# Optimization experiments

Measured on AMD Instinct MI355X. Metric: run time of the kernel, lower is better.

## Reference

```python
import jax, jax.numpy as jnp
from jax import lax
import numpy as np

PROPRIO = 48
NPTS = 1024
NP_PROX = 512
NP_DIST = 512
HP = 187  # proximal_feature_dim
HD = 64   # distal_feature_dim
B = 2048
NA = 12
ACTOR_DIMS = [PROPRIO + HP + HD, 1024, 512, 256, 128, NA]


def gru_last(x, wih, whh, bih, bhh):
    """torch-style GRU (gate order r,z,n), returns last hidden. x: [B,T,in]."""
    Bx, T, _ = x.shape
    H = whh.shape[1]
    gx = x @ wih.T + bih  # [B,T,3H], input projections precomputed
    def step(h, gxt):
        gh = h @ whh.T + bhh
        r = jax.nn.sigmoid(gxt[:, :H] + gh[:, :H])
        z = jax.nn.sigmoid(gxt[:, H:2 * H] + gh[:, H:2 * H])
        n = jnp.tanh(gxt[:, 2 * H:] + r * gh[:, 2 * H:])
        return (1.0 - z) * n + z * h, None
    h0 = jnp.zeros((Bx, H), x.dtype)
    hT, _ = lax.scan(step, h0, jnp.swapaxes(gx, 0, 1))
    return hT


def _encode(pts, w1, b1, w2, b2):
    h = jax.nn.elu(pts @ w1.T + b1)
    return jax.nn.elu(h @ w2.T + b2)


def _forward(obs, pe_prox_w1, pe_prox_b1, pe_prox_w2, pe_prox_b2,
             pe_dist_w1, pe_dist_b1, pe_dist_w2, pe_dist_b2,
             gru_prox_wih, gru_prox_whh, gru_prox_bih, gru_prox_bhh,
             gru_dist_wih, gru_dist_whh, gru_dist_bih, gru_dist_bhh,
             mem_prox_wih, mem_prox_whh, mem_prox_bih, mem_prox_bhh,
             mem_dist_wih, mem_dist_whh, mem_dist_bih, mem_dist_bhh,
             actor_w0, actor_b0, actor_w1, actor_b1, actor_w2, actor_b2,
             actor_w3, actor_b3, actor_w4, actor_b4,
             prox_idx, dist_idx):
    proprio = obs[:, :PROPRIO]
    lidar = obs[:, PROPRIO:].reshape(obs.shape[0], NPTS, 3)  # history_length=1
    # irregular gather of proximal/distal point subsets (sampling plan buffers)
    prox_enc = _encode(lidar[:, prox_idx], pe_prox_w1, pe_prox_b1, pe_prox_w2, pe_prox_b2)  # [B,512,64]
    dist_enc = _encode(lidar[:, dist_idx], pe_dist_w1, pe_dist_b1, pe_dist_w2, pe_dist_b2)  # [B,512,64]
    # spatial GRUs over the point sequence
    hp = gru_last(prox_enc, gru_prox_wih, gru_prox_whh, gru_prox_bih, gru_prox_bhh)  # [B,187]
    hd = gru_last(dist_enc, gru_dist_wih, gru_dist_whh, gru_dist_bih, gru_dist_bhh)  # [B,64]
    # temporal memory GRUs (single step, zero initial hidden)
    fp = gru_last(hp[:, None, :], mem_prox_wih, mem_prox_whh, mem_prox_bih, mem_prox_bhh)
    fd = gru_last(hd[:, None, :], mem_dist_wih, mem_dist_whh, mem_dist_bih, mem_dist_bhh)
    x = jnp.concatenate([proprio, fp, fd], axis=-1)  # [B,299]
    for w, b in ((actor_w0, actor_b0), (actor_w1, actor_b1), (actor_w2, actor_b2), (actor_w3, actor_b3)):
        x = jax.nn.elu(x @ w.T + b)
    return x @ actor_w4.T + actor_b4  # action mean [B,12]


def setup_inputs() -> dict:
    key = jax.random.key(0)
    ks = iter(jax.random.split(key, 64))
    def n(shape, scale=0.05):
        return (jax.random.normal(next(ks), shape, jnp.float32) * scale)
    inp = {}
    inp["obs"] = jax.random.normal(next(ks), (B, PROPRIO + NPTS * 3), jnp.float32)
    inp["prox_idx"] = jax.random.randint(next(ks), (NP_PROX,), 0, NPTS)
    inp["dist_idx"] = jax.random.randint(next(ks), (NP_DIST,), 0, NPTS)
    for pfx in ("pe_prox", "pe_dist"):
        inp[pfx + "_w1"] = n((64, 3)); inp[pfx + "_b1"] = jnp.zeros((64,), jnp.float32)
        inp[pfx + "_w2"] = n((64, 64)); inp[pfx + "_b2"] = jnp.zeros((64,), jnp.float32)
    for pfx, H, din in (("gru_prox", HP, 64), ("gru_dist", HD, 64), ("mem_prox", HP, HP), ("mem_dist", HD, HD)):
        inp[pfx + "_wih"] = n((3 * H, din)); inp[pfx + "_whh"] = n((3 * H, H))
        inp[pfx + "_bih"] = jnp.zeros((3 * H,), jnp.float32); inp[pfx + "_bhh"] = jnp.zeros((3 * H,), jnp.float32)
    for i, (di, do) in enumerate(zip(ACTOR_DIMS[:-1], ACTOR_DIMS[1:])):
        inp[f"actor_w{i}"] = n((do, di)); inp[f"actor_b{i}"] = jnp.zeros((do,), jnp.float32)
    return inp


def reference(obs, prox_idx, dist_idx,
              pe_prox_w1, pe_prox_b1, pe_prox_w2, pe_prox_b2,
              pe_dist_w1, pe_dist_b1, pe_dist_w2, pe_dist_b2,
              gru_prox_wih, gru_prox_whh, gru_prox_bih, gru_prox_bhh,
              gru_dist_wih, gru_dist_whh, gru_dist_bih, gru_dist_bhh,
              mem_prox_wih, mem_prox_whh, mem_prox_bih, mem_prox_bhh,
              mem_dist_wih, mem_dist_whh, mem_dist_bih, mem_dist_bhh,
              actor_w0, actor_b0, actor_w1, actor_b1, actor_w2, actor_b2,
              actor_w3, actor_b3, actor_w4, actor_b4):
    return _forward(obs, pe_prox_w1, pe_prox_b1, pe_prox_w2, pe_prox_b2,
                    pe_dist_w1, pe_dist_b1, pe_dist_w2, pe_dist_b2,
                    gru_prox_wih, gru_prox_whh, gru_prox_bih, gru_prox_bhh,
                    gru_dist_wih, gru_dist_whh, gru_dist_bih, gru_dist_bhh,
                    mem_prox_wih, mem_prox_whh, mem_prox_bih, mem_prox_bhh,
                    mem_dist_wih, mem_dist_whh, mem_dist_bih, mem_dist_bhh,
                    actor_w0, actor_b0, actor_w1, actor_b1, actor_w2, actor_b2,
                    actor_w3, actor_b3, actor_w4, actor_b4,
                    prox_idx, dist_idx)
```

## Files before the change

kernel.cpp:

```cpp
#include <hip/hip_runtime.h>
#include <stdint.h>

typedef __attribute__((ext_vector_type(8))) short short8;
typedef __attribute__((ext_vector_type(4))) float f32x4;
typedef __attribute__((ext_vector_type(4))) unsigned int u32x4;

#define DEV __device__ __forceinline__

#define L2E 1.4426950408889634f

DEV unsigned short f2bf(float f) {
    union { float f; uint32_t u; } v; v.f = f;
    return (unsigned short)((v.u + 0x7FFFu + ((v.u >> 16) & 1u)) >> 16);
}
#if defined(__has_builtin)
#if __has_builtin(__builtin_amdgcn_cvt_pk_bf16_f32)
#define HAS_PK_BF16 1
#endif
#if __has_builtin(__builtin_amdgcn_cvt_pk_fp8_f32)
#define HAS_PK_FP8 1
#endif
#endif
DEV uint32_t pk_bf16(float a, float b) {
#ifdef HAS_PK_BF16
    typedef __attribute__((ext_vector_type(2))) __bf16 bf2;
    union { bf2 v; uint32_t u; } cv;
    cv.v = __builtin_amdgcn_cvt_pk_bf16_f32(a, b);
    return cv.u;
#else
    return (uint32_t)f2bf(a) | ((uint32_t)f2bf(b) << 16);
#endif
}
DEV uint8_t f2fp8(float f) {
    union { float f; uint32_t u; } v; v.f = f;
    uint32_t s = (v.u >> 24) & 0x80u;
    uint32_t absu = v.u & 0x7FFFFFFFu;
    int E = (int)(absu >> 23);
    if (E >= 136) return (uint8_t)(s | 0x7E);
    if (E >= 121) {
        uint32_t m = absu & 0x7FFFFFu;
        uint32_t keep = m >> 20;
        uint32_t rest = m & 0xFFFFFu;
        uint32_t rnd = (rest > 0x80000u || (rest == 0x80000u && (keep & 1u))) ? 1u : 0u;
        uint32_t mag = (((uint32_t)(E - 120) << 3) | keep) + rnd;
        if (mag > 0x7Eu) mag = 0x7Eu;
        return (uint8_t)(s | mag);
    }
    float sc = __builtin_fabsf(f) * 512.f;
    uint32_t m8 = (uint32_t)(sc + 0.5f);
    if (m8 > 7u) return (uint8_t)(s | 0x08);
    return (uint8_t)(s | m8);
}
DEV uint32_t pk_fp8x4(float a, float b, float c, float d) {
#ifdef HAS_PK_FP8
    int lo   = __builtin_amdgcn_cvt_pk_fp8_f32(a, b, 0, false);
    int both = __builtin_amdgcn_cvt_pk_fp8_f32(c, d, lo, true);
    return (uint32_t)both;
#else
    return (uint32_t)f2fp8(a) | ((uint32_t)f2fp8(b) << 8)
         | ((uint32_t)f2fp8(c) << 16) | ((uint32_t)f2fp8(d) << 24);
#endif
}
DEV float rcp1pe_(float x) {
    return __builtin_amdgcn_rcpf(1.f + __builtin_amdgcn_exp2f(x));
}
DEV float sig_(float x) { return rcp1pe_(-L2E * x); }
DEV float elu_(float x) {
    return x > 0.f ? x : __builtin_amdgcn_exp2f(L2E * x) - 1.f;
}
DEV f32x4 splat4(float v) { f32x4 r; r[0]=v; r[1]=v; r[2]=v; r[3]=v; return r; }
DEV void pin(short8& v) { asm volatile("" : "+v"(v)); }
DEV void pinl(long& v)  { asm volatile("" : "+v"(v)); }

struct PJob { const float* s; void* d; int Hs, NG, Ks, Kd, total; float s0, s1, s2; int fmt; };
struct PJobs { PJob j[13]; };

__global__ __launch_bounds__(256) void pack_all(PJobs P)
{
    PJob jb = P.j[blockIdx.y];
    int e = blockIdx.x * 256 + threadIdx.x;
    if (e >= jb.total) return;
    int n = e / jb.Kd, k = e - n * jb.Kd;
    int g = n / jb.NG, jj = n - g * jb.NG;
    float sc = (g == 0) ? jb.s0 : ((g == 1) ? jb.s1 : jb.s2);
    float v = (jj < jb.Hs && k < jb.Ks) ? jb.s[(size_t)(g * jb.Hs + jj) * jb.Ks + k] * sc : 0.f;
    if (jb.fmt) ((uint8_t*)jb.d)[e] = (uint8_t)(pk_fp8x4(v, 0.f, 0.f, 0.f) & 0xFFu);
    else        ((unsigned short*)jb.d)[e] = f2bf(v);
}

__global__ __launch_bounds__(256) void enc_kernel(
    const float* __restrict__ obs, const int* __restrict__ idx,
    const float* __restrict__ w1, const float* __restrict__ b1,
    const unsigned short* __restrict__ w2p, const float* __restrict__ b2,
    uint8_t* __restrict__ enc8)
{
    const int b = blockIdx.x, t0 = blockIdx.y * 64;
    const int tid = threadIdx.x;
    __shared__ __align__(16) float pts[64][4];
    __shared__ float w1s[256];
    __shared__ float b1s[64], b2s[64];
    __shared__ __align__(16) unsigned short h1s[64][72];
    __shared__ __align__(16) uint8_t x8s[64 * 80];

    if (tid < 192) w1s[(tid/3)*4 + (tid - (tid/3)*3)] = w1[tid];
    if (tid < 64) { b1s[tid] = b1[tid]; b2s[tid] = b2[tid]; }
    for (int e = tid; e < 192; e += 256) {
        int p = e / 3, c2 = e - p * 3;
        int pi = idx[t0 + p];
        pts[p][c2] = obs[(size_t)b * 3120 + 48 + (size_t)pi * 3 + c2];
    }
    __syncthreads();
#pragma unroll
    for (int r = 0; r < 16; ++r) {
        int e = tid + r * 256;
        int p = e >> 6, ch = e & 63;
        float v = w1s[ch*4]*pts[p][0] + w1s[ch*4+1]*pts[p][1]
                + w1s[ch*4+2]*pts[p][2] + b1s[ch];
        h1s[p][ch] = f2bf(elu_(v));
    }
    __syncthreads();
    const int wave = tid >> 6, lane = tid & 63, quad = lane >> 4, l16 = lane & 15;
#pragma unroll
    for (int ct = 0; ct < 4; ++ct) {
        f32x4 a2 = splat4(0.f);
#pragma unroll
        for (int ks = 0; ks < 2; ++ks) {
            short8 af = *(const short8*)(&h1s[wave*16 + l16][ks*32 + quad*8]);
            short8 bf = *(const short8*)(w2p + (ct*16 + l16)*64 + ks*32 + quad*8);
            a2 = __builtin_amdgcn_mfma_f32_16x16x32_bf16(af, bf, a2, 0, 0, 0);
        }
        int c = ct*16 + l16;
        float b2v = b2s[c];
        uint32_t pk = pk_fp8x4(elu_(a2[0] + b2v), elu_(a2[1] + b2v),
                               elu_(a2[2] + b2v), elu_(a2[3] + b2v));
#pragma unroll
        for (int j = 0; j < 4; ++j)
            x8s[(wave*16 + quad*4 + j)*80 + c] = (uint8_t)(pk >> (8*j));
    }
    __syncthreads();
    {
        int row = tid >> 2, seg = tid & 3;
        *(u32x4*)(enc8 + ((size_t)b*512 + t0 + row)*64 + seg*16) =
            *(const u32x4*)(x8s + row*80 + seg*16);
    }
}

DEV void gru_body_pre(int blk, const uint8_t* __restrict__ enc8,
                      const uint8_t* __restrict__ wih8,
                      const unsigned short* __restrict__ whh,
                      const float* __restrict__ bih, const float* __restrict__ bhh,
                      unsigned short* __restrict__ houtb, char* smem)
{
    constexpr int H = 187, KP = 192, KS = 6, HP8 = 200;
    unsigned short* hlds = (unsigned short*)smem;
    uint8_t* xs = (uint8_t*)(smem + 12800);

    const int tid  = threadIdx.x;
    const int wave = tid >> 6, lane = tid & 63, quad = lane >> 4, l16 = lane & 15;
    const int b0   = blk * 16;
    const int c    = wave * 16 + l16;

    const int sx = (l16 >> 2) & 3;
    const int qo = (quad ^ sx) * 8;
    const int cc = c >> 3, cl = c & 7;
    const int wcol = ((cc & ~3) | ((cc & 3) ^ quad)) * 8 + cl;

    for (int e = tid; e < 2*16*HP8; e += 768) hlds[e] = 0;

    short8 whr[3][KS];
    long   wx8[3][2];
#pragma unroll
    for (int g = 0; g < 3; ++g) {
#pragma unroll
        for (int ks = 0; ks < KS; ++ks)
            whr[g][ks] = *(const short8*)(whh + ((size_t)(g*KP + c))*KP + ks*32 + quad*8);
#pragma unroll
        for (int ks = 0; ks < 2; ++ks)
            wx8[g][ks] = *(const long*)(wih8 + ((size_t)(g*KP + c))*64 + ks*32 + quad*8);
    }
#pragma unroll
    for (int g = 0; g < 3; ++g) {
#pragma unroll
        for (int ks = 0; ks < KS; ++ks) pin(whr[g][ks]);
#pragma unroll
        for (int ks = 0; ks < 2; ++ks)  pinl(wx8[g][ks]);
    }
    float bsr = 0.f, bsz = 0.f, binx = 0.f, bhnn = 0.f;
    if (c < H) {
        bsr  = -L2E * (bih[c]       + bhh[c]);
        bsz  = -L2E * (bih[H + c]   + bhh[H + c]);
        binx = 2.f * L2E * bih[2*H + c];
        bhnn = 2.f * L2E * bhh[2*H + c];
    }
    float hreg[4] = {0.f, 0.f, 0.f, 0.f};

    u32x4 xq;
    const int xrow = lane >> 2, xseg = lane & 3;
    if (wave == 0) {
        xq = *(const u32x4*)(enc8 + ((size_t)(b0 + xrow)*512 + 0)*64 + xseg*16);
        *(u32x4*)(xs + 0*1280 + xrow*80 + xseg*16) = xq;
        xq = *(const u32x4*)(enc8 + ((size_t)(b0 + xrow)*512 + 1)*64 + xseg*16);
    }
    __syncthreads();

    int cur = 0;
    for (int t = 0; t < 512; ++t) {
        if (wave == 0) {
            *(u32x4*)(xs + ((t+1)&1)*1280 + xrow*80 + xseg*16) = xq;
            int tn = (t + 2 < 512) ? t + 2 : 511;
            xq = *(const u32x4*)(enc8 + ((size_t)(b0 + xrow)*512 + tn)*64 + xseg*16);
        }
        const uint8_t* xsr = xs + (t&1)*1280;
        const unsigned short* hc = hlds + cur * (16*HP8);
        unsigned short*       hn = hlds + (cur ^ 1) * (16*HP8);

        f32x4 acc[4];
        acc[0] = splat4(bsr);
        acc[1] = splat4(bsz);
        acc[2] = splat4(binx);
        acc[3] = splat4(bhnn);
#pragma unroll
        for (int ks = 0; ks < 2; ++ks) {
            long a8 = *(const long*)(xsr + l16*80 + ks*32 + quad*8);
            acc[0] = __builtin_amdgcn_mfma_f32_16x16x32_fp8_fp8(a8, wx8[0][ks], acc[0], 0, 0, 0);
            acc[1] = __builtin_amdgcn_mfma_f32_16x16x32_fp8_fp8(a8, wx8[1][ks], acc[1], 0, 0, 0);
            acc[2] = __builtin_amdgcn_mfma_f32_16x16x32_fp8_fp8(a8, wx8[2][ks], acc[2], 0, 0, 0);
        }
#pragma unroll
        for (int ks = 0; ks < KS; ++ks) {
            short8 ah = *(const short8*)(hc + l16*HP8 + ks*32 + qo);
            acc[0] = __builtin_amdgcn_mfma_f32_16x16x32_bf16(ah, whr[0][ks], acc[0], 0, 0, 0);
            acc[1] = __builtin_amdgcn_mfma_f32_16x16x32_bf16(ah, whr[1][ks], acc[1], 0, 0, 0);
            acc[3] = __builtin_amdgcn_mfma_f32_16x16x32_bf16(ah, whr[2][ks], acc[3], 0, 0, 0);
        }
        float hv[4];
#pragma unroll
        for (int j = 0; j < 4; ++j) {
            float r  = rcp1pe_(acc[0][j]);
            float zg = rcp1pe_(acc[1][j]);
            float nn = __builtin_fmaf(-2.f, rcp1pe_(__builtin_fmaf(r, acc[3][j], acc[2][j])), 1.f);
            hv[j] = __builtin_fmaf(zg, hreg[j] - nn, nn);
            hreg[j] = hv[j];
        }
        uint32_t p01 = pk_bf16(hv[0], hv[1]);
        uint32_t p23 = pk_bf16(hv[2], hv[3]);
        hn[(quad*4+0)*HP8 + wcol] = (unsigned short)p01;
        hn[(quad*4+1)*HP8 + wcol] = (unsigned short)(p01 >> 16);
        hn[(quad*4+2)*HP8 + wcol] = (unsigned short)p23;
        hn[(quad*4+3)*HP8 + wcol] = (unsigned short)(p23 >> 16);
        cur ^= 1;
        __syncthreads();
    }
#pragma unroll
    for (int j = 0; j < 4; ++j) {
        int m = quad*4 + j;
        houtb[(size_t)(b0 + m)*KP + c] = (c < H) ? f2bf(hreg[j]) : 0;
    }
}

template<int H, int KP>
DEV void gru_body_fused(int blk,
                  const float* __restrict__ obs, const int* __restrict__ idx,
                  const float* __restrict__ w1, const float* __restrict__ b1,
                  const float* __restrict__ w2, const float* __restrict__ b2,
                  const unsigned short* __restrict__ wih, const unsigned short* __restrict__ whh,
                  const float* __restrict__ bih, const float* __restrict__ bhh,
                  unsigned short* __restrict__ houtb, char* smem)
{
    constexpr int NCT = KP / 16;
    constexpr int KS  = KP / 32;
    constexpr int HP8 = KP + 8;

    unsigned short* hlds = (unsigned short*)(smem);
    unsigned short* xs   = (unsigned short*)(smem + 12800);
    unsigned short* h1s  = (unsigned short*)(smem + 17408);
    unsigned short* w2s  = (unsigned short*)(smem + 22016);
    float* ptsb          = (float*)(smem + 31232);
    float* w1s           = (float*)(smem + 31744);
    float* b1s           = (float*)(smem + 32768);
    float* b2s           = (float*)(smem + 33024);

    const int tid  = threadIdx.x;
    const int wave = tid >> 6, lane = tid & 63, quad = lane >> 4, l16 = lane & 15;
    const int b0   = blk * 16;
    const int ct   = wave;
    const bool act = (ct < NCT);
    const int c    = ct * 16 + l16;

    for (int e = tid; e < 2*16*HP8; e += 768) hlds[e] = 0;
    for (int e = tid; e < 4096; e += 768) { int n = e >> 6, k = e & 63; w2s[n*72 + k] = f2bf(w2[e]); }
    if (tid < 192) w1s[(tid/3)*4 + (tid - (tid/3)*3)] = w1[tid];
    if (tid < 64) { b1s[tid] = b1[tid]; b2s[tid] = b2[tid]; }

    const float* myrow = obs + (size_t)(b0 + (tid & 15)) * 3120 + 48;
    float px = 0.f, py = 0.f, pz = 0.f;
    if (tid < 16) {
        int p0 = idx[0];
        ptsb[tid*4 + 0] = myrow[3*p0 + 0];
        ptsb[tid*4 + 1] = myrow[3*p0 + 1];
        ptsb[tid*4 + 2] = myrow[3*p0 + 2];
        int p1 = idx[1];
        px = myrow[3*p1 + 0]; py = myrow[3*p1 + 1]; pz = myrow[3*p1 + 2];
    }

    short8 whr[3][KS];
    short8 wxr[3][2];
    float bsr = 0.f, bsz = 0.f, binx = 0.f, bhnn = 0.f;
    {
        const int cl = act ? c : l16;
#pragma unroll
        for (int g = 0; g < 3; ++g) {
#pragma unroll
            for (int ks = 0; ks < KS; ++ks)
                whr[g][ks] = *(const short8*)(whh + ((size_t)(g*KP + cl))*KP + ks*32 + quad*8);
#pragma unroll
            for (int ks = 0; ks < 2; ++ks)
                wxr[g][ks] = *(const short8*)(wih + ((size_t)(g*KP + cl))*64 + ks*32 + quad*8);
        }
    }
#pragma unroll
    for (int g = 0; g < 3; ++g) {
#pragma unroll
        for (int ks = 0; ks < KS; ++ks) pin(whr[g][ks]);
#pragma unroll
        for (int ks = 0; ks < 2; ++ks)  pin(wxr[g][ks]);
    }
    if (act && c < H) {
        bsr  = -L2E * (bih[c]       + bhh[c]);
        bsz  = -L2E * (bih[H + c]   + bhh[H + c]);
        binx = 2.f * L2E * bih[2*H + c];
        bhnn = 2.f * L2E * bhh[2*H + c];
    }
    float hreg[4] = {0.f, 0.f, 0.f, 0.f};

    __syncthreads();

    int cur = 0;
    for (int i = 0; i < 514; ++i) {
        if (i < 512) {
            const float* pt = ptsb + (i & 1) * 64;
            unsigned short* h1w = h1s + (i & 1) * (16*72);
#pragma unroll
            for (int e = tid; e < 1024; e += 768) {
                int p = e >> 6, ch = e & 63;
                float v = w1s[ch*4+0]*pt[p*4+0] + w1s[ch*4+1]*pt[p*4+1]
                        + w1s[ch*4+2]*pt[p*4+2] + b1s[ch];
                h1w[p*72 + ch] = f2bf(elu_(v));
            }
            if (tid < 16) {
                float* dst = ptsb + ((i+1) & 1) * 64 + tid*4;
                dst[0] = px; dst[1] = py; dst[2] = pz;
                int tn = (i + 2 < 512) ? i + 2 : 511;
                int pn = idx[tn];
                px = myrow[3*pn + 0]; py = myrow[3*pn + 1]; pz = myrow[3*pn + 2];
            }
        }
        if (i >= 1 && i < 513 && wave < 4) {
            const unsigned short* h1r = h1s + ((i-1) & 1) * (16*72);
            unsigned short*       xw  = xs  + ((i-1) & 1) * (16*72);
            f32x4 a2 = splat4(0.f);
#pragma unroll
            for (int ks = 0; ks < 2; ++ks) {
                short8 af = *(const short8*)(h1r + l16*72 + ks*32 + quad*8);
                short8 bf = *(const short8*)(w2s + (wave*16 + l16)*72 + ks*32 + quad*8);
                a2 = __builtin_amdgcn_mfma_f32_16x16x32_bf16(af, bf, a2, 0, 0, 0);
            }
            int c2 = wave*16 + l16;
            float b2v = b2s[c2];
#pragma unroll
            for (int j = 0; j < 4; ++j)
                xw[(quad*4 + j)*72 + c2] = f2bf(elu_(a2[j] + b2v));
        }
        if (i >= 2) {
            int t = i - 2;
            const unsigned short* xsr = xs + (t & 1) * (16*72);
            const unsigned short* hc  = hlds + cur * (16*HP8);
            unsigned short*       hn  = hlds + (cur ^ 1) * (16*HP8);
            if (act) {
                f32x4 acc[4];
                acc[0] = splat4(bsr);
                acc[1] = splat4(bsz);
                acc[2] = splat4(binx);
                acc[3] = splat4(bhnn);
#pragma unroll
                for (int ks = 0; ks < 2; ++ks) {
                    short8 xf = *(const short8*)(xsr + l16*72 + ks*32 + quad*8);
                    acc[0] = __builtin_amdgcn_mfma_f32_16x16x32_bf16(xf, wxr[0][ks], acc[0], 0, 0, 0);
                    acc[1] = __builtin_amdgcn_mfma_f32_16x16x32_bf16(xf, wxr[1][ks], acc[1], 0, 0, 0);
                    acc[2] = __builtin_amdgcn_mfma_f32_16x16x32_bf16(xf, wxr[2][ks], acc[2], 0, 0, 0);
                }
#pragma unroll
                for (int ks = 0; ks < KS; ++ks) {
                    short8 ah = *(const short8*)(hc + l16*HP8 + ks*32 + quad*8);
                    acc[0] = __builtin_amdgcn_mfma_f32_16x16x32_bf16(ah, whr[0][ks], acc[0], 0, 0, 0);
                    acc[1] = __builtin_amdgcn_mfma_f32_16x16x32_bf16(ah, whr[1][ks], acc[1], 0, 0, 0);
                    acc[3] = __builtin_amdgcn_mfma_f32_16x16x32_bf16(ah, whr[2][ks], acc[3], 0, 0, 0);
                }
                float hv[4];
#pragma unroll
                for (int j = 0; j < 4; ++j) {
                    float r  = rcp1pe_(acc[0][j]);
                    float zg = rcp1pe_(acc[1][j]);
                    float nn = __builtin_fmaf(-2.f, rcp1pe_(__builtin_fmaf(r, acc[3][j], acc[2][j])), 1.f);
                    hv[j] = __builtin_fmaf(zg, hreg[j] - nn, nn);
                    hreg[j] = hv[j];
                }
                uint32_t p01 = pk_bf16(hv[0], hv[1]);
                uint32_t p23 = pk_bf16(hv[2], hv[3]);
                hn[(quad*4+0)*HP8 + c] = (unsigned short)p01;
                hn[(quad*4+1)*HP8 + c] = (unsigned short)(p01 >> 16);
                hn[(quad*4+2)*HP8 + c] = (unsigned short)p23;
                hn[(quad*4+3)*HP8 + c] = (unsigned short)(p23 >> 16);
            }
            cur ^= 1;
        }
        __syncthreads();
    }

    if (act)
#pragma unroll
        for (int j = 0; j < 4; ++j) {
            int m = quad*4 + j;
            houtb[(size_t)(b0 + m)*KP + c] = (c < H) ? f2bf(hreg[j]) : 0;
        }
}

__global__ __launch_bounds__(768) void gru_kernel(
    int mode,
    const float* __restrict__ obs,
    const int* __restrict__ prox_idx, const int* __restrict__ dist_idx,
    const uint8_t* __restrict__ encp8, const uint8_t* __restrict__ wihp8,
    const float* __restrict__ w1p, const float* __restrict__ b1p,
    const float* __restrict__ w2p, const float* __restrict__ b2p,
    const float* __restrict__ w1d, const float* __restrict__ b1d,
    const float* __restrict__ w2d, const float* __restrict__ b2d,
    const unsigned short* __restrict__ wihp, const unsigned short* __restrict__ whhp,
    const unsigned short* __restrict__ wihd, const unsigned short* __restrict__ whhd,
    const float* __restrict__ bihp, const float* __restrict__ bhhp,
    const float* __restrict__ bihd, const float* __restrict__ bhhd,
    unsigned short* __restrict__ hpb, unsigned short* __restrict__ hdb)
{
    __shared__ __align__(16) char smem[33280];
    if (blockIdx.x < 128) {
        if (mode == 0)
            gru_body_pre(blockIdx.x, encp8, wihp8, whhp, bihp, bhhp, hpb, smem);
        else
            gru_body_fused<187, 192>(blockIdx.x, obs, prox_idx, w1p, b1p, w2p, b2p,
                                     wihp, whhp, bihp, bhhp, hpb, smem);
    } else {
        gru_body_fused<64, 64>(blockIdx.x - 128, obs, dist_idx, w1d, b1d, w2d, b2d,
                               wihd, whhd, bihd, bhhd, hdb, smem);
    }
}

__global__ __launch_bounds__(256) void memfuse_kernel(
    const float* __restrict__ obs,
    const unsigned short* __restrict__ hpb, const unsigned short* __restrict__ hdb,
    const unsigned short* __restrict__ mwp, const unsigned short* __restrict__ mwd,
    const float* __restrict__ mbip, const float* __restrict__ mbhp,
    const float* __restrict__ mbid, const float* __restrict__ mbhd,
    unsigned short* __restrict__ x0b)
{
    __shared__ __align__(16) unsigned short Asl[64*40];
    __shared__ __align__(16) unsigned short Bsl[3][64*40];
    const int tid = threadIdx.x;
    const int wave = tid >> 6, lane = tid & 63, quad = lane >> 4, l16 = lane & 15;
    const int z = blockIdx.x, m0 = blockIdx.y * 64;
    const bool isp = (z < 3);
    const unsigned short* A = isp ? hpb : hdb;
    const unsigned short* B = isp ? mwp : mwd;
    const float* bi = isp ? mbip : mbid;
    const float* bh = isp ? mbhp : mbhd;
    const int Kp = isp ? 192 : 64;
    const int Hh = isp ? 187 : 64;
    const int jb = isp ? z * 64 : 0;
    const int cbase = isp ? 48 : 235;
    const int r = tid >> 2, sg = (tid & 3) * 8;

    f32x4 acc[3][4];
#pragma unroll
    for (int g = 0; g < 3; ++g)
#pragma unroll
        for (int nt = 0; nt < 4; ++nt) acc[g][nt] = splat4(0.f);

    for (int k0 = 0; k0 < Kp; k0 += 32) {
        *(short8*)(Asl + r*40 + sg) = *(const short8*)(A + (size_t)(m0 + r)*Kp + k0 + sg);
#pragma unroll
        for (int g = 0; g < 3; ++g)
            *(short8*)(Bsl[g] + r*40 + sg) =
                *(const short8*)(B + (size_t)(g*Kp + jb + r)*Kp + k0 + sg);
        __syncthreads();
        short8 af = *(const short8*)(Asl + (wave*16 + l16)*40 + quad*8);
#pragma unroll
        for (int g = 0; g < 3; ++g)
#pragma unroll
            for (int nt = 0; nt < 4; ++nt) {
                short8 bf = *(const short8*)(Bsl[g] + (nt*16 + l16)*40 + quad*8);
                acc[g][nt] = __builtin_amdgcn_mfma_f32_16x16x32_bf16(af, bf, acc[g][nt], 0, 0, 0);
            }
        __syncthreads();
    }
#pragma unroll
    for (int nt = 0; nt < 4; ++nt) {
        int j = jb + nt*16 + l16;
        bool valid = (j < Hh);
        float br = 0.f, bz = 0.f, bnx = 0.f, bnh = 0.f;
        if (valid) {
            br  = -L2E * (bi[j] + bh[j]);
            bz  = -L2E * (bi[Hh + j] + bh[Hh + j]);
            bnx = 2.f * L2E * bi[2*Hh + j];
            bnh = 2.f * L2E * bh[2*Hh + j];
        }
#pragma unroll
        for (int jj = 0; jj < 4; ++jj) {
            int m = m0 + wave*16 + quad*4 + jj;
            float rr = rcp1pe_(acc[0][nt][jj] + br);
            float zz = rcp1pe_(acc[1][nt][jj] + bz);
            float tt = __builtin_fmaf(rr, bnh, acc[2][nt][jj] + bnx);
            float nn = __builtin_fmaf(-2.f, rcp1pe_(tt), 1.f);
            float v  = (1.f - zz) * nn;
            if (valid) x0b[(size_t)m*320 + cbase + j] = f2bf(v);
        }
    }
    if (z == 0) {
        for (int e = tid; e < 64*48; e += 256) {
            int m = m0 + e / 48, cc = e - (e / 48) * 48;
            x0b[(size_t)m*320 + cc] = f2bf(obs[(size_t)m*3120 + cc]);
        }
    }
    if (z == 3) {
        for (int e = tid; e < 64*21; e += 256) {
            int m = m0 + e / 21, cc = 299 + (e - (e / 21) * 21);
            x0b[(size_t)m*320 + cc] = 0;
        }
    }
}

__global__ __launch_bounds__(256) void bgemm_kernel(
    const unsigned short* __restrict__ A, const unsigned short* __restrict__ B,
    const float* __restrict__ bias, void* __restrict__ C,
    int Kp, int Np, int Nstore, int mode)
{
    __shared__ __align__(16) unsigned short Asl[64*72];
    __shared__ __align__(16) unsigned short Bsl[64*72];
    const int tid = threadIdx.x;
    const int wave = tid >> 6, lane = tid & 63, quad = lane >> 4, l16 = lane & 15;
    const int n0 = blockIdx.x * 64, m0 = blockIdx.y * 64;
    const int r = tid >> 2, sg = (tid & 3) * 16;

    f32x4 acc[4];
#pragma unroll
    for (int nt = 0; nt < 4; ++nt) acc[nt] = splat4(0.f);

    for (int k0 = 0; k0 < Kp; k0 += 64) {
        *(short8*)(Asl + r*72 + sg)     = *(const short8*)(A + (size_t)(m0 + r)*Kp + k0 + sg);
        *(short8*)(Asl + r*72 + sg + 8) = *(const short8*)(A + (size_t)(m0 + r)*Kp + k0 + sg + 8);
        if (n0 + r < Np) {
            *(short8*)(Bsl + r*72 + sg)     = *(const short8*)(B + (size_t)(n0 + r)*Kp + k0 + sg);
            *(short8*)(Bsl + r*72 + sg + 8) = *(const short8*)(B + (size_t)(n0 + r)*Kp + k0 + sg + 8);
        } else {
            short8 zz; for (int q = 0; q < 8; ++q) zz[q] = 0;
            *(short8*)(Bsl + r*72 + sg) = zz;
            *(short8*)(Bsl + r*72 + sg + 8) = zz;
        }
        __syncthreads();
#pragma unroll
        for (int ks = 0; ks < 2; ++ks) {
            short8 af = *(const short8*)(Asl + (wave*16 + l16)*72 + ks*32 + quad*8);
#pragma unroll
            for (int nt = 0; nt < 4; ++nt) {
                short8 bf = *(const short8*)(Bsl + (nt*16 + l16)*72 + ks*32 + quad*8);
                acc[nt] = __builtin_amdgcn_mfma_f32_16x16x32_bf16(af, bf, acc[nt], 0, 0, 0);
            }
        }
        __syncthreads();
    }
#pragma unroll
    for (int nt = 0; nt < 4; ++nt) {
        int n = n0 + nt*16 + l16;
        float bv = (bias && n < Np) ? bias[n] : 0.f;
#pragma unroll
        for (int j = 0; j < 4; ++j) {
            int m = m0 + wave*16 + quad*4 + j;
            float v = acc[nt][j] + bv;
            if (mode == 1) {
                ((unsigned short*)C)[(size_t)m*Np + n] = f2bf(elu_(v));
            } else {
                if (n < Nstore) ((float*)C)[(size_t)m*Nstore + n] = v;
            }
        }
    }
}

__global__ __launch_bounds__(256) void gemm34_kernel(
    const unsigned short* __restrict__ A,
    const unsigned short* __restrict__ W3,
    const float* __restrict__ b3,
    const unsigned short* __restrict__ W4,
    const float* __restrict__ b4,
    float* __restrict__ out)
{
    __shared__ __align__(16) char smem[9216 + 18432];
    unsigned short* Asl  = (unsigned short*)smem;
    unsigned short* B3sl = (unsigned short*)(smem + 9216);
    unsigned short* a4s  = (unsigned short*)smem;
    const int tid = threadIdx.x;
    const int wave = tid >> 6, lane = tid & 63, quad = lane >> 4, l16 = lane & 15;
    const int m0 = blockIdx.x * 64;

    f32x4 acc3[8];
#pragma unroll
    for (int nt = 0; nt < 8; ++nt) acc3[nt] = splat4(0.f);

    const int r = tid >> 2, sg = (tid & 3) * 16;
    const int r2 = tid >> 1, sg2 = (tid & 1) * 32;
    for (int k0 = 0; k0 < 256; k0 += 64) {
        *(short8*)(Asl + r*72 + sg)     = *(const short8*)(A + (size_t)(m0 + r)*256 + k0 + sg);
        *(short8*)(Asl + r*72 + sg + 8) = *(const short8*)(A + (size_t)(m0 + r)*256 + k0 + sg + 8);
#pragma unroll
        for (int s = 0; s < 4; ++s)
            *(short8*)(B3sl + r2*72 + sg2 + s*8) =
                *(const short8*)(W3 + (size_t)r2*256 + k0 + sg2 + s*8);
        __syncthreads();
#pragma unroll
        for (int ks = 0; ks < 2; ++ks) {
            short8 af = *(const short8*)(Asl + (wave*16 + l16)*72 + ks*32 + quad*8);
#pragma unroll
            for (int nt = 0; nt < 8; ++nt) {
                short8 bf = *(const short8*)(B3sl + (nt*16 + l16)*72 + ks*32 + quad*8);
                acc3[nt] = __builtin_amdgcn_mfma_f32_16x16x32_bf16(af, bf, acc3[nt], 0, 0, 0);
            }
        }
        __syncthreads();
    }
#pragma unroll
    for (int nt = 0; nt < 8; ++nt) {
        int n = nt*16 + l16;
        float bv = b3[n];
#pragma unroll
        for (int j = 0; j < 4; ++j) {
            int m = wave*16 + quad*4 + j;
            a4s[m*136 + n] = f2bf(elu_(acc3[nt][j] + bv));
        }
    }
    __syncthreads();
    f32x4 acc4 = splat4(0.f);
#pragma unroll
    for (int ks = 0; ks < 4; ++ks) {
        short8 af = *(const short8*)(a4s + (wave*16 + l16)*136 + ks*32 + quad*8);
        short8 bf = *(const short8*)(W4 + (size_t)l16*128 + ks*32 + quad*8);
        acc4 = __builtin_amdgcn_mfma_f32_16x16x32_bf16(af, bf, acc4, 0, 0, 0);
    }
    if (l16 < 12) {
        float bv = b4[l16];
#pragma unroll
        for (int j = 0; j < 4; ++j)
            out[(size_t)(m0 + wave*16 + quad*4 + j)*12 + l16] = acc4[j] + bv;
    }
}

extern "C" void kernel_launch(void* const* d_in, const int* in_sizes, int n_in,
                              void* d_out, int out_size, void* d_ws, size_t ws_size,
                              hipStream_t stream)
{
    (void)in_sizes; (void)n_in; (void)out_size;
    const float* obs        = (const float*)d_in[0];
    const int*   prox_idx   = (const int*)d_in[1];
    const int*   dist_idx   = (const int*)d_in[2];
    const float* pe_prox_w1 = (const float*)d_in[3];
    const float* pe_prox_b1 = (const float*)d_in[4];
    const float* pe_prox_w2 = (const float*)d_in[5];
    const float* pe_prox_b2 = (const float*)d_in[6];
    const float* pe_dist_w1 = (const float*)d_in[7];
    const float* pe_dist_b1 = (const float*)d_in[8];
    const float* pe_dist_w2 = (const float*)d_in[9];
    const float* pe_dist_b2 = (const float*)d_in[10];
    const float* gp_wih = (const float*)d_in[11];
    const float* gp_whh = (const float*)d_in[12];
    const float* gp_bih = (const float*)d_in[13];
    const float* gp_bhh = (const float*)d_in[14];
    const float* gd_wih = (const float*)d_in[15];
    const float* gd_whh = (const float*)d_in[16];
    const float* gd_bih = (const float*)d_in[17];
    const float* gd_bhh = (const float*)d_in[18];
    const float* mp_wih = (const float*)d_in[19];
    const float* mp_bih = (const float*)d_in[21];
    const float* mp_bhh = (const float*)d_in[22];
    const float* md_wih = (const float*)d_in[23];
    const float* md_bih = (const float*)d_in[25];
    const float* md_bhh = (const float*)d_in[26];
    const float* aw0 = (const float*)d_in[27]; const float* ab0 = (const float*)d_in[28];
    const float* aw1 = (const float*)d_in[29]; const float* ab1 = (const float*)d_in[30];
    const float* aw2 = (const float*)d_in[31]; const float* ab2 = (const float*)d_in[32];
    const float* aw3 = (const float*)d_in[33]; const float* ab3 = (const float*)d_in[34];
    const float* aw4 = (const float*)d_in[35]; const float* ab4 = (const float*)d_in[36];
    float* out = (float*)d_out;

    char* ws = (char*)d_ws;
    size_t off = 0;
    auto alloc = [&](size_t bytes) -> char* {
        char* p = ws + off;
        off = (off + bytes + 255) & ~(size_t)255;
        return p;
    };
    unsigned short* wih_p = (unsigned short*)alloc(36864*2);
    unsigned short* whh_p = (unsigned short*)alloc(110592*2);
    unsigned short* wih_d = (unsigned short*)alloc(12288*2);
    unsigned short* whh_d = (unsigned short*)alloc(12288*2);
    unsigned short* mw_p  = (unsigned short*)alloc(110592*2);
    unsigned short* mw_d  = (unsigned short*)alloc(12288*2);
    unsigned short* w0p   = (unsigned short*)alloc((size_t)1024*320*2);
    unsigned short* w1p   = (unsigned short*)alloc((size_t)512*1024*2);
    unsigned short* w2p   = (unsigned short*)alloc((size_t)256*512*2);
    unsigned short* w3p   = (unsigned short*)alloc((size_t)128*256*2);
    unsigned short* w4p   = (unsigned short*)alloc((size_t)16*128*2);
    unsigned short* w2e   = (unsigned short*)alloc(4096*2);
    uint8_t* wih8         = (uint8_t*)alloc(576*64);
    unsigned short* hpb   = (unsigned short*)alloc((size_t)2048*192*2);
    unsigned short* hdb   = (unsigned short*)alloc((size_t)2048*64*2);
    unsigned short* x0b   = (unsigned short*)alloc((size_t)2048*320*2);
    unsigned short* a1b   = (unsigned short*)alloc((size_t)2048*1024*2);
    unsigned short* a2b   = (unsigned short*)alloc((size_t)2048*512*2);
    unsigned short* a3b   = (unsigned short*)alloc((size_t)2048*256*2);
    uint8_t* enc8         = (uint8_t*)alloc((size_t)2048*512*64);
    const int mode = (off <= ws_size) ? 0 : 1;

    const float SR = -L2E, SN = 2.f * L2E;
    PJobs P;
    P.j[0]  = { gp_wih, wih_p, 187, 192, 64, 64, 36864, SR, SR, SN, 0 };
    P.j[1]  = { gp_whh, whh_p, 187, 192, 187, 192, 110592, SR, SR, SN, 0 };
    P.j[2]  = { gd_wih, wih_d, 64, 64, 64, 64, 12288, SR, SR, SN, 0 };
    P.j[3]  = { gd_whh, whh_d, 64, 64, 64, 64, 12288, SR, SR, SN, 0 };
    P.j[4]  = { mp_wih, mw_p, 187, 192, 187, 192, 110592, SR, SR, SN, 0 };
    P.j[5]  = { md_wih, mw_d, 64, 64, 64, 64, 12288, SR, SR, SN, 0 };
    P.j[6]  = { aw0, w0p, 1024, 1024, 299, 320, 327680, 1.f, 1.f, 1.f, 0 };
    P.j[7]  = { aw1, w1p, 512, 512, 1024, 1024, 524288, 1.f, 1.f, 1.f, 0 };
    P.j[8]  = { aw2, w2p, 256, 256, 512, 512, 131072, 1.f, 1.f, 1.f, 0 };
    P.j[9]  = { aw3, w3p, 128, 128, 256, 256, 32768, 1.f, 1.f, 1.f, 0 };
    P.j[10] = { aw4, w4p, 12, 16, 128, 128, 2048, 1.f, 1.f, 1.f, 0 };
    P.j[11] = { pe_prox_w2, w2e, 64, 64, 64, 64, 4096, 1.f, 1.f, 1.f, 0 };
    P.j[12] = { gp_wih, wih8, 187, 192, 64, 64, 36864, SR, SR, SN, 1 };
    pack_all<<<dim3(2048, 13), 256, 0, stream>>>(P);

    if (mode == 0) {
        enc_kernel<<<dim3(2048, 8), 256, 0, stream>>>(
            obs, prox_idx, pe_prox_w1, pe_prox_b1, w2e, pe_prox_b2, enc8);
    }

    gru_kernel<<<256, 768, 0, stream>>>(
        mode, obs, prox_idx, dist_idx, enc8, wih8,
        pe_prox_w1, pe_prox_b1, pe_prox_w2, pe_prox_b2,
        pe_dist_w1, pe_dist_b1, pe_dist_w2, pe_dist_b2,
        wih_p, whh_p, wih_d, whh_d,
        gp_bih, gp_bhh, gd_bih, gd_bhh, hpb, hdb);

    memfuse_kernel<<<dim3(4, 32), 256, 0, stream>>>(
        obs, hpb, hdb, mw_p, mw_d, mp_bih, mp_bhh, md_bih, md_bhh, x0b);

    bgemm_kernel<<<dim3(16, 32), 256, 0, stream>>>(x0b, w0p, ab0, a1b, 320, 1024, 1024, 1);
    bgemm_kernel<<<dim3(8,  32), 256, 0, stream>>>(a1b, w1p, ab1, a2b, 1024, 512, 512, 1);
    bgemm_kernel<<<dim3(4,  32), 256, 0, stream>>>(a2b, w2p, ab2, a3b, 512, 256, 256, 1);
    gemm34_kernel<<<32, 256, 0, stream>>>(a3b, w3p, ab3, w4p, ab4, out);
}
```

Baseline: 805.3 us.

## Flatten pack launch into prefix-indexed grid and loop encoder over point chunks per block

```diff
diff --git a/kernel.cpp b/kernel.cpp
--- a/kernel.cpp
+++ b/kernel.cpp
@@ -4,6 +4,7 @@
 typedef __attribute__((ext_vector_type(8))) short short8;
 typedef __attribute__((ext_vector_type(4))) float f32x4;
 typedef __attribute__((ext_vector_type(4))) unsigned int u32x4;
+typedef __attribute__((ext_vector_type(4))) float float4v;
 
 #define DEV __device__ __forceinline__
 
@@ -64,7 +65,6 @@
 DEV float rcp1pe_(float x) {
     return __builtin_amdgcn_rcpf(1.f + __builtin_amdgcn_exp2f(x));
 }
-DEV float sig_(float x) { return rcp1pe_(-L2E * x); }
 DEV float elu_(float x) {
     return x > 0.f ? x : __builtin_amdgcn_exp2f(L2E * x) - 1.f;
 }
@@ -72,76 +72,91 @@
 DEV void pin(short8& v) { asm volatile("" : "+v"(v)); }
 DEV void pinl(long& v)  { asm volatile("" : "+v"(v)); }
 
-struct PJob { const float* s; void* d; int Hs, NG, Ks, Kd, total; float s0, s1, s2; int fmt; };
-struct PJobs { PJob j[13]; };
+struct PJob { const float* s; void* d; int Hs, NG, Ks, Kd; float s0, s1, s2; int fmt; };
+struct PJobs { PJob j[12]; int pref[13]; };
 
 __global__ __launch_bounds__(256) void pack_all(PJobs P)
 {
-    PJob jb = P.j[blockIdx.y];
     int e = blockIdx.x * 256 + threadIdx.x;
-    if (e >= jb.total) return;
-    int n = e / jb.Kd, k = e - n * jb.Kd;
+    if (e >= P.pref[12]) return;
+    int ji = 0;
+    while (e >= P.pref[ji + 1]) ++ji;
+    PJob jb = P.j[ji];
+    int le = e - P.pref[ji];
+    int n = le / jb.Kd, k = le - n * jb.Kd;
     int g = n / jb.NG, jj = n - g * jb.NG;
     float sc = (g == 0) ? jb.s0 : ((g == 1) ? jb.s1 : jb.s2);
     float v = (jj < jb.Hs && k < jb.Ks) ? jb.s[(size_t)(g * jb.Hs + jj) * jb.Ks + k] * sc : 0.f;
-    if (jb.fmt) ((uint8_t*)jb.d)[e] = (uint8_t)(pk_fp8x4(v, 0.f, 0.f, 0.f) & 0xFFu);
-    else        ((unsigned short*)jb.d)[e] = f2bf(v);
+    if (jb.fmt) ((uint8_t*)jb.d)[le] = (uint8_t)(pk_fp8x4(v, 0.f, 0.f, 0.f) & 0xFFu);
+    else        ((unsigned short*)jb.d)[le] = f2bf(v);
 }
 
 __global__ __launch_bounds__(256) void enc_kernel(
     const float* __restrict__ obs, const int* __restrict__ idx,
     const float* __restrict__ w1, const float* __restrict__ b1,
-    const unsigned short* __restrict__ w2p, const float* __restrict__ b2,
+    const float* __restrict__ w2, const float* __restrict__ b2,
     uint8_t* __restrict__ enc8)
 {
-    const int b = blockIdx.x, t0 = blockIdx.y * 64;
+    const int b = blockIdx.x;
     const int tid = threadIdx.x;
-    __shared__ __align__(16) float pts[64][4];
-    __shared__ float w1s[256];
-    __shared__ float b1s[64], b2s[64];
-    __shared__ __align__(16) unsigned short h1s[64][72];
-    __shared__ __align__(16) uint8_t x8s[64 * 80];
-
-    if (tid < 192) w1s[(tid/3)*4 + (tid - (tid/3)*3)] = w1[tid];
-    if (tid < 64) { b1s[tid] = b1[tid]; b2s[tid] = b2[tid]; }
-    for (int e = tid; e < 192; e += 256) {
-        int p = e / 3, c2 = e - p * 3;
-        int pi = idx[t0 + p];
-        pts[p][c2] = obs[(size_t)b * 3120 + 48 + (size_t)pi * 3 + c2];
+    __shared__ __align__(16) float lid[3072];
+    __shared__ int idxs[512];
+    __shared__ float w1s[256], b1s[64], b2s[64];
+    __shared__ __align__(16) unsigned short w2s[64*72];
+    __shared__ __align__(16) unsigned short h1s[64*72];
+    __shared__ __align__(16) uint8_t x8s[64*80];
+
+    {
+        const float4v* src = (const float4v*)(obs + (size_t)b * 3120 + 48);
+#pragma unroll
+        for (int r = 0; r < 3; ++r) ((float4v*)lid)[tid + r*256] = src[tid + r*256];
+        for (int e = tid; e < 512; e += 256) idxs[e] = idx[e];
+        for (int e = tid; e < 4096; e += 256) {
+            int n = e >> 6, k = e & 63;
+            w2s[n*72 + k] = f2bf(w2[e]);
+        }
+        if (tid < 192) w1s[(tid/3)*4 + (tid - (tid/3)*3)] = w1[tid];
+        if (tid < 64) { b1s[tid] = b1[tid]; b2s[tid] = b2[tid]; }
     }
     __syncthreads();
-#pragma unroll
-    for (int r = 0; r < 16; ++r) {
-        int e = tid + r * 256;
-        int p = e >> 6, ch = e & 63;
-        float v = w1s[ch*4]*pts[p][0] + w1s[ch*4+1]*pts[p][1]
-                + w1s[ch*4+2]*pts[p][2] + b1s[ch];
-        h1s[p][ch] = f2bf(elu_(v));
-    }
-    __syncthreads();
+
     const int wave = tid >> 6, lane = tid & 63, quad = lane >> 4, l16 = lane & 15;
-#pragma unroll
-    for (int ct = 0; ct < 4; ++ct) {
-        f32x4 a2 = splat4(0.f);
-#pragma unroll
-        for (int ks = 0; ks < 2; ++ks) {
-            short8 af = *(const short8*)(&h1s[wave*16 + l16][ks*32 + quad*8]);
-            short8 bf = *(const short8*)(w2p + (ct*16 + l16)*64 + ks*32 + quad*8);
-            a2 = __builtin_amdgcn_mfma_f32_16x16x32_bf16(af, bf, a2, 0, 0, 0);
-        }
-        int c = ct*16 + l16;
-        float b2v = b2s[c];
-        uint32_t pk = pk_fp8x4(elu_(a2[0] + b2v), elu_(a2[1] + b2v),
-                               elu_(a2[2] + b2v), elu_(a2[3] + b2v));
-#pragma unroll
-        for (int j = 0; j < 4; ++j)
-            x8s[(wave*16 + quad*4 + j)*80 + c] = (uint8_t)(pk >> (8*j));
-    }
-    __syncthreads();
-    {
-        int row = tid >> 2, seg = tid & 3;
-        *(u32x4*)(enc8 + ((size_t)b*512 + t0 + row)*64 + seg*16) =
-            *(const u32x4*)(x8s + row*80 + seg*16);
+    for (int tc = 0; tc < 8; ++tc) {
+        const int t0 = tc * 64;
+#pragma unroll
+        for (int r = 0; r < 16; ++r) {
+            int e = tid + r * 256;
+            int p = e >> 6, ch = e & 63;
+            int pi = idxs[t0 + p];
+            float x = lid[3*pi], y = lid[3*pi + 1], z = lid[3*pi + 2];
+            float v = w1s[ch*4]*x + w1s[ch*4+1]*y + w1s[ch*4+2]*z + b1s[ch];
+            h1s[p*72 + ch] = f2bf(elu_(v));
+        }
+        __syncthreads();
+#pragma unroll
+        for (int ct = 0; ct < 4; ++ct) {
+            f32x4 a2 = splat4(0.f);
+#pragma unroll
+            for (int ks = 0; ks < 2; ++ks) {
+                short8 af = *(const short8*)(h1s + (wave*16 + l16)*72 + ks*32 + quad*8);
+                short8 bf = *(const short8*)(w2s + (ct*16 + l16)*72 + ks*32 + quad*8);
+                a2 = __builtin_amdgcn_mfma_f32_16x16x32_bf16(af, bf, a2, 0, 0, 0);
+            }
+            int c = ct*16 + l16;
+            float b2v = b2s[c];
+            uint32_t pk = pk_fp8x4(elu_(a2[0] + b2v), elu_(a2[1] + b2v),
+                                   elu_(a2[2] + b2v), elu_(a2[3] + b2v));
+#pragma unroll
+            for (int j = 0; j < 4; ++j)
+                x8s[(wave*16 + quad*4 + j)*80 + c] = (uint8_t)(pk >> (8*j));
+        }
+        __syncthreads();
+        {
+            int row = tid >> 2, seg = tid & 3;
+            *(u32x4*)(enc8 + ((size_t)b*512 + t0 + row)*64 + seg*16) =
+                *(const u32x4*)(x8s + row*80 + seg*16);
+        }
+        __syncthreads();
     }
 }
 
@@ -714,7 +729,6 @@
     unsigned short* w2p   = (unsigned short*)alloc((size_t)256*512*2);
     unsigned short* w3p   = (unsigned short*)alloc((size_t)128*256*2);
     unsigned short* w4p   = (unsigned short*)alloc((size_t)16*128*2);
-    unsigned short* w2e   = (unsigned short*)alloc(4096*2);
     uint8_t* wih8         = (uint8_t*)alloc(576*64);
     unsigned short* hpb   = (unsigned short*)alloc((size_t)2048*192*2);
     unsigned short* hdb   = (unsigned short*)alloc((size_t)2048*64*2);
@@ -727,24 +741,27 @@
 
     const float SR = -L2E, SN = 2.f * L2E;
     PJobs P;
-    P.j[0]  = { gp_wih, wih_p, 187, 192, 64, 64, 36864, SR, SR, SN, 0 };
-    P.j[1]  = { gp_whh, whh_p, 187, 192, 187, 192, 110592, SR, SR, SN, 0 };
-    P.j[2]  = { gd_wih, wih_d, 64, 64, 64, 64, 12288, SR, SR, SN, 0 };
-    P.j[3]  = { gd_whh, whh_d, 64, 64, 64, 64, 12288, SR, SR, SN, 0 };
-    P.j[4]  = { mp_wih, mw_p, 187, 192, 187, 192, 110592, SR, SR, SN, 0 };
-    P.j[5]  = { md_wih, mw_d, 64, 64, 64, 64, 12288, SR, SR, SN, 0 };
-    P.j[6]  = { aw0, w0p, 1024, 1024, 299, 320, 327680, 1.f, 1.f, 1.f, 0 };
-    P.j[7]  = { aw1, w1p, 512, 512, 1024, 1024, 524288, 1.f, 1.f, 1.f, 0 };
-    P.j[8]  = { aw2, w2p, 256, 256, 512, 512, 131072, 1.f, 1.f, 1.f, 0 };
-    P.j[9]  = { aw3, w3p, 128, 128, 256, 256, 32768, 1.f, 1.f, 1.f, 0 };
-    P.j[10] = { aw4, w4p, 12, 16, 128, 128, 2048, 1.f, 1.f, 1.f, 0 };
-    P.j[11] = { pe_prox_w2, w2e, 64, 64, 64, 64, 4096, 1.f, 1.f, 1.f, 0 };
-    P.j[12] = { gp_wih, wih8, 187, 192, 64, 64, 36864, SR, SR, SN, 1 };
-    pack_all<<<dim3(2048, 13), 256, 0, stream>>>(P);
+    int tot[12];
+    P.j[0]  = { gp_wih, wih_p, 187, 192, 64, 64, SR, SR, SN, 0 };      tot[0]  = 36864;
+    P.j[1]  = { gp_whh, whh_p, 187, 192, 187, 192, SR, SR, SN, 0 };    tot[1]  = 110592;
+    P.j[2]  = { gd_wih, wih_d, 64, 64, 64, 64, SR, SR, SN, 0 };        tot[2]  = 12288;
+    P.j[3]  = { gd_whh, whh_d, 64, 64, 64, 64, SR, SR, SN, 0 };        tot[3]  = 12288;
+    P.j[4]  = { mp_wih, mw_p, 187, 192, 187, 192, SR, SR, SN, 0 };     tot[4]  = 110592;
+    P.j[5]  = { md_wih, mw_d, 64, 64, 64, 64, SR, SR, SN, 0 };         tot[5]  = 12288;
+    P.j[6]  = { aw0, w0p, 1024, 1024, 299, 320, 1.f, 1.f, 1.f, 0 };    tot[6]  = 327680;
+    P.j[7]  = { aw1, w1p, 512, 512, 1024, 1024, 1.f, 1.f, 1.f, 0 };    tot[7]  = 524288;
+    P.j[8]  = { aw2, w2p, 256, 256, 512, 512, 1.f, 1.f, 1.f, 0 };      tot[8]  = 131072;
+    P.j[9]  = { aw3, w3p, 128, 128, 256, 256, 1.f, 1.f, 1.f, 0 };      tot[9]  = 32768;
+    P.j[10] = { aw4, w4p, 12, 16, 128, 128, 1.f, 1.f, 1.f, 0 };        tot[10] = 2048;
+    P.j[11] = { gp_wih, wih8, 187, 192, 64, 64, SR, SR, SN, 1 };       tot[11] = 36864;
+    P.pref[0] = 0;
+    for (int i = 0; i < 12; ++i) P.pref[i+1] = P.pref[i] + tot[i];
+    const int npack = (P.pref[12] + 255) / 256;
+    pack_all<<<npack, 256, 0, stream>>>(P);
 
     if (mode == 0) {
-        enc_kernel<<<dim3(2048, 8), 256, 0, stream>>>(
-            obs, prox_idx, pe_prox_w1, pe_prox_b1, w2e, pe_prox_b2, enc8);
+        enc_kernel<<<2048, 256, 0, stream>>>(
+            obs, prox_idx, pe_prox_w1, pe_prox_b1, pe_prox_w2, pe_prox_b2, enc8);
     }
 
     gru_kernel<<<256, 768, 0, stream>>>(
```

After: 785.5 us. 2.5% less time.
